# Optimization experiments

Measured on AMD Instinct MI355X. Metric: run time of the kernel, lower is better.

The kernel has to match this reference:

```python
import jax, jax.numpy as jnp
import numpy as np

B, H, S, D = 2, 16, 2048, 64

def setup_inputs() -> dict:
    key = jax.random.key(0)
    kq, kk, kv = jax.random.split(key, 3)
    q = jax.random.normal(kq, (B, H, S, D), dtype=jnp.float32)
    k = jax.random.normal(kk, (B, H, S, D), dtype=jnp.float32)
    v = jax.random.normal(kv, (B, H, S, D), dtype=jnp.float32)
    # causal mask: True where position j > i (future tokens are masked)
    mask = jnp.triu(jnp.ones((S, S), dtype=bool), k=1)[None, None, :, :]
    return {"q": q, "k": k, "v": v, "mask": mask}

def reference(q, k, v, mask) -> jnp.ndarray:
    # scaled dot-product attention with additive -1e4 mask bias
    scale = 1.0 / jnp.sqrt(jnp.asarray(q.shape[-1], q.dtype))
    scores = jnp.einsum('bhqd,bhkd->bhqk', q, k) * scale  # [B,H,S,S]
    scores = scores + mask.astype(scores.dtype) * jnp.asarray(-10000.0, scores.dtype)
    probs = jax.nn.softmax(scores, axis=-1)
    # dropout is identity in eval mode
    return jnp.einsum('bhqk,bhkd->bhqd', probs, v)
```

## Files before the change

kernel.cpp:

```cpp
#include <hip/hip_runtime.h>

typedef __bf16 bf16_t;
typedef bf16_t bf16x2 __attribute__((ext_vector_type(2)));
typedef bf16_t bf16x4 __attribute__((ext_vector_type(4)));
typedef bf16_t bf16x8 __attribute__((ext_vector_type(8)));
typedef float  floatx16 __attribute__((ext_vector_type(16)));
typedef unsigned int uintx4 __attribute__((ext_vector_type(4)));

constexpr int Sq = 2048, Dq = 64;
constexpr int BQ = 128;
constexpr int KVB = 64;
constexpr int NQT = Sq / BQ;
constexpr float SCALE_LOG2E = 0.125f * 1.44269504088896340736f;

struct LoopS { bf16_t K[2][2][KVB * Dq]; bf16_t V[2][2][Dq * KVB]; };
struct EpiS  { float Op[BQ][Dq]; float den[BQ]; };
union  SmemU { LoopS l; EpiS e; };

static __device__ __forceinline__ bf16x8 cvt8(const float4& a, const float4& b) {
    bf16x8 w;
    w[0] = (bf16_t)a.x; w[1] = (bf16_t)a.y; w[2] = (bf16_t)a.z; w[3] = (bf16_t)a.w;
    w[4] = (bf16_t)b.x; w[5] = (bf16_t)b.y; w[6] = (bf16_t)b.z; w[7] = (bf16_t)b.w;
    return w;
}
static __device__ __forceinline__ bf16x8 cvt8s(const float4& a, const float4& b) {
    bf16x8 w;
    w[0] = (bf16_t)(a.x * SCALE_LOG2E); w[1] = (bf16_t)(a.y * SCALE_LOG2E);
    w[2] = (bf16_t)(a.z * SCALE_LOG2E); w[3] = (bf16_t)(a.w * SCALE_LOG2E);
    w[4] = (bf16_t)(b.x * SCALE_LOG2E); w[5] = (bf16_t)(b.y * SCALE_LOG2E);
    w[6] = (bf16_t)(b.z * SCALE_LOG2E); w[7] = (bf16_t)(b.w * SCALE_LOG2E);
    return w;
}
static __device__ __forceinline__ unsigned int pkbf(float lo, float hi) {
    bf16x2 t; t[0] = (bf16_t)lo; t[1] = (bf16_t)hi;
    return __builtin_bit_cast(unsigned int, t);
}

#define SUM16(p) (((((p)[0]+(p)[1])+((p)[2]+(p)[3]))+(((p)[4]+(p)[5])+((p)[6]+(p)[7]))) \
                + ((((p)[8]+(p)[9])+((p)[10]+(p)[11]))+(((p)[12]+(p)[13])+((p)[14]+(p)[15]))))

#define LOADKV(kt) do {                                                        \
    const long kb_ = base + (long)(kt) * KVB * Dq;                             \
    const float* ks_ = &K[kb_ + (long)krow_st * Dq + kd0];                     \
    kr0 = *(const float4*)&ks_[0];  kr1 = *(const float4*)&ks_[4];             \
    kr2 = *(const float4*)&ks_[8];  kr3 = *(const float4*)&ks_[12];            \
    _Pragma("unroll")                                                          \
    for (int p_ = 0; p_ < 4; ++p_) {                                           \
        const int j0_ = vjw + 4 * ((p_ + vh) & 3);                             \
        _Pragma("unroll")                                                      \
        for (int r_ = 0; r_ < 4; ++r_)                                         \
            vraw[p_][r_] = V[kb_ + (long)(j0_ + r_) * Dq + vd];                \
    } } while (0)

#define WRITEKV(kdst, vdst) do {                                               \
    char* kc_ = (char*)(kdst) + krow_st * 128;                                 \
    const int ksw_ = (krow_st & 7) << 4;                                       \
    *(bf16x8*)(kc_ + ((2 * kd0) ^ ksw_))      = cvt8(kr0, kr1);                \
    *(bf16x8*)(kc_ + ((2 * kd0 + 16) ^ ksw_)) = cvt8(kr2, kr3);                \
    char* vc_ = (char*)(vdst) + vd * 128;                                      \
    const int vsw_ = (vd & 7) << 4;                                            \
    _Pragma("unroll")                                                          \
    for (int p_ = 0; p_ < 4; ++p_) {                                           \
        const int j0_ = vjw + 4 * ((p_ + vh) & 3);                             \
        bf16x4 vw_;                                                            \
        vw_[0] = (bf16_t)vraw[p_][0]; vw_[1] = (bf16_t)vraw[p_][1];            \
        vw_[2] = (bf16_t)vraw[p_][2]; vw_[3] = (bf16_t)vraw[p_][3];            \
        *(bf16x4*)(vc_ + ((2 * j0_) ^ vsw_)) = vw_;                            \
    } } while (0)

__global__ __launch_bounds__(512, 2) void flash_attn_kernel(
    const float* __restrict__ Q, const float* __restrict__ K,
    const float* __restrict__ V, float* __restrict__ O)
{
    __shared__ SmemU sm;

    const int tid  = threadIdx.x;
    const int grp  = tid >> 8;
    const int gtid = tid & 255;
    const int wave = gtid >> 6;
    const int lane = gtid & 63;
    const int hi   = lane >> 5;
    const int l31  = lane & 31;

    const int id = blockIdx.x;
    const int bh = (id & 7) + ((id >> 6) << 3);
    const int pr = (id >> 3) & 7;
    const long base = (long)bh * Sq * Dq;

    const int krow_st = gtid >> 2;
    const int kd0     = 16 * (gtid & 3);
    const int vd      = gtid & 63;
    const int vjw     = 16 * (gtid >> 6);
    const int vh      = (gtid & 63) >> 3;

    bf16_t* const Kb0 = &sm.l.K[grp][0][0];
    bf16_t* const Kb1 = &sm.l.K[grp][1][0];
    bf16_t* const Vb0 = &sm.l.V[grp][0][0];
    bf16_t* const Vb1 = &sm.l.V[grp][1][0];
    const int lsw = (l31 & 7) << 4;

    for (int half = 0; half < 2; ++half) {
        const int qt = half ? (NQT - 1 - pr) : pr;
        const long qb = base + (long)qt * BQ * Dq;
        const int qrow = 32 * wave + l31;
        const int niter = qt + 1;

        bf16x8 qf[4];
        #pragma unroll
        for (int ss = 0; ss < 4; ++ss) {
            const float* qp = &Q[qb + (long)qrow * Dq + 16 * ss + 8 * hi];
            qf[ss] = cvt8s(*(const float4*)&qp[0], *(const float4*)&qp[4]);
        }

        float4 kr0, kr1, kr2, kr3;
        float  vraw[4][4];

        __syncthreads();
        LOADKV(grp);
        WRITEKV(Kb0, Vb0);
        __syncthreads();

        float l_lane = 0.f;
        floatx16 oacc[2];
        oacc[0] = (floatx16)0.f; oacc[1] = (floatx16)0.f;

        for (int i = 0; i < niter; ++i) {
            const int kt = 2 * i + grp;
            const bool more = (i + 1 < niter);
            if (more) LOADKV(kt + 2);

            if (64 * kt <= BQ * qt + 32 * wave + 31) {
                const bf16_t* kbase = (i & 1) ? Kb1 : Kb0;
                const bf16_t* vbase = (i & 1) ? Vb1 : Vb0;

                floatx16 s0 = (floatx16)0.f, s1 = (floatx16)0.f;
                __builtin_amdgcn_s_setprio(1);
                #pragma unroll
                for (int ss = 0; ss < 4; ++ss) {
                    const int cb = (32 * ss + 16 * hi) ^ lsw;
                    bf16x8 k0 = *(const bf16x8*)((const char*)kbase + l31 * 128 + cb);
                    bf16x8 k1 = *(const bf16x8*)((const char*)kbase + (32 + l31) * 128 + cb);
                    s0 = __builtin_amdgcn_mfma_f32_32x32x16_bf16(k0, qf[ss], s0, 0, 0, 0);
                    s1 = __builtin_amdgcn_mfma_f32_32x32x16_bf16(k1, qf[ss], s1, 0, 0, 0);
                }
                __builtin_amdgcn_s_setprio(0);

                float p0[16], p1[16];
                const bool diag = (kt >= 2 * qt);
                const int kg0 = 64 * kt;
                const int qg  = BQ * qt + qrow;
                #pragma unroll
                for (int r = 0; r < 16; ++r) {
                    const int cr = (r & 3) + 8 * (r >> 2) + 4 * hi;
                    float a = s0[r], b = s1[r];
                    if (diag) {
                        if (kg0 + cr > qg)      a = -1e30f;
                        if (kg0 + 32 + cr > qg) b = -1e30f;
                    }
                    p0[r] = __builtin_amdgcn_exp2f(a);
                    p1[r] = __builtin_amdgcn_exp2f(b);
                }
                l_lane += SUM16(p0) + SUM16(p1);

                unsigned int w[4][4];
                #pragma unroll
                for (int s = 0; s < 4; ++s) {
                    const float* pt = (s >> 1) ? p1 : p0;
                    const int R = 8 * (s & 1);
                    unsigned int c0 = pkbf(pt[R + 0], pt[R + 1]);
                    unsigned int c1 = pkbf(pt[R + 2], pt[R + 3]);
                    unsigned int d0 = pkbf(pt[R + 4], pt[R + 5]);
                    unsigned int d1 = pkbf(pt[R + 6], pt[R + 7]);
                    asm volatile("v_permlane32_swap_b32 %0, %1" : "+v"(c0), "+v"(d0));
                    asm volatile("v_permlane32_swap_b32 %0, %1" : "+v"(c1), "+v"(d1));
                    w[s][0] = c0; w[s][1] = c1; w[s][2] = d0; w[s][3] = d1;
                }

                __builtin_amdgcn_s_setprio(1);
                #pragma unroll
                for (int t2 = 0; t2 < 2; ++t2) {
                    #pragma unroll
                    for (int s = 0; s < 4; ++s) {
                        uintx4 fw; fw[0] = w[s][0]; fw[1] = w[s][1];
                        fw[2] = w[s][2]; fw[3] = w[s][3];
                        const bf16x8 pa = __builtin_bit_cast(bf16x8, fw);
                        const int cb = (32 * s + 16 * hi) ^ lsw;
                        bf16x8 vf = *(const bf16x8*)((const char*)vbase + (32 * t2 + l31) * 128 + cb);
                        oacc[t2] = __builtin_amdgcn_mfma_f32_32x32x16_bf16(pa, vf, oacc[t2], 0, 0, 0);
                    }
                }
                __builtin_amdgcn_s_setprio(0);
            }

            if (more) WRITEKV((i & 1) ? Kb0 : Kb1, (i & 1) ? Vb0 : Vb1);
            __syncthreads();
        }

        const float lden = l_lane + __shfl_xor(l_lane, 32);

        if (grp == 1) {
            #pragma unroll
            for (int t2 = 0; t2 < 2; ++t2)
                #pragma unroll
                for (int r = 0; r < 16; ++r) {
                    const int cr = (r & 3) + 8 * (r >> 2) + 4 * hi;
                    sm.e.Op[32 * wave + cr][32 * t2 + l31] = oacc[t2][r];
                }
            if (hi == 0) sm.e.den[32 * wave + l31] = lden;
        }
        __syncthreads();
        if (grp == 0) {
            #pragma unroll
            for (int r = 0; r < 16; ++r) {
                const int cr = (r & 3) + 8 * (r >> 2) + 4 * hi;
                const float dA = __shfl(lden, cr);
                const float dB = sm.e.den[32 * wave + cr];
                const float inv = 1.f / (dA + dB);
                const long orow = qb + (long)(32 * wave + cr) * Dq;
                #pragma unroll
                for (int t2 = 0; t2 < 2; ++t2) {
                    const float ov = oacc[t2][r] + sm.e.Op[32 * wave + cr][32 * t2 + l31];
                    O[orow + 32 * t2 + l31] = ov * inv;
                }
            }
        }
    }
}

extern "C" void kernel_launch(void* const* d_in, const int* in_sizes, int n_in,
                              void* d_out, int out_size, void* d_ws, size_t ws_size,
                              hipStream_t stream)
{
    const float* q = (const float*)d_in[0];
    const float* k = (const float*)d_in[1];
    const float* v = (const float*)d_in[2];
    float* out = (float*)d_out;
    flash_attn_kernel<<<dim3(256, 1, 1), dim3(512, 1, 1), 0, stream>>>(q, k, v, out);
}
```

Measured before the change: 143.8 us.

## Halve query and KV tile sizes and double grid with padded V layout

Shrinks the query tile from 128 to 64 rows and the KV tile from 64 to 32, launching 512 blocks of 256 threads instead of 256 blocks of 512. V is now stored transposed in shared memory with an 80-byte padded row stride instead of the XOR swizzle, so each thread writes 16 contiguous bf16 values with two vector stores. The aim is more blocks for load balance across CUs and a simpler V staging path. The cost is lower per-block MFMA reuse, twice as many barriers per unit of work, and less work between synchronisations.

```diff
diff --git a/kernel.cpp b/kernel.cpp
--- a/kernel.cpp
+++ b/kernel.cpp
@@ -2,18 +2,19 @@
 
 typedef __bf16 bf16_t;
 typedef bf16_t bf16x2 __attribute__((ext_vector_type(2)));
-typedef bf16_t bf16x4 __attribute__((ext_vector_type(4)));
 typedef bf16_t bf16x8 __attribute__((ext_vector_type(8)));
 typedef float  floatx16 __attribute__((ext_vector_type(16)));
 typedef unsigned int uintx4 __attribute__((ext_vector_type(4)));
 
 constexpr int Sq = 2048, Dq = 64;
-constexpr int BQ = 128;
-constexpr int KVB = 64;
+constexpr int BQ = 64;
+constexpr int KVB = 32;
 constexpr int NQT = Sq / BQ;
 constexpr float SCALE_LOG2E = 0.125f * 1.44269504088896340736f;
-
-struct LoopS { bf16_t K[2][2][KVB * Dq]; bf16_t V[2][2][Dq * KVB]; };
+constexpr int KROW_B = 128;
+constexpr int VROW_B = 80;
+
+struct LoopS { char Kl[2][2][KVB * KROW_B]; char Vl[2][2][Dq * VROW_B]; };
 struct EpiS  { float Op[BQ][Dq]; float den[BQ]; };
 union  SmemU { LoopS l; EpiS e; };
 
@@ -39,160 +40,148 @@
 #define SUM16(p) (((((p)[0]+(p)[1])+((p)[2]+(p)[3]))+(((p)[4]+(p)[5])+((p)[6]+(p)[7]))) \
                 + ((((p)[8]+(p)[9])+((p)[10]+(p)[11]))+(((p)[12]+(p)[13])+((p)[14]+(p)[15]))))
 
-#define LOADKV(kt) do {                                                        \
-    const long kb_ = base + (long)(kt) * KVB * Dq;                             \
-    const float* ks_ = &K[kb_ + (long)krow_st * Dq + kd0];                     \
-    kr0 = *(const float4*)&ks_[0];  kr1 = *(const float4*)&ks_[4];             \
-    kr2 = *(const float4*)&ks_[8];  kr3 = *(const float4*)&ks_[12];            \
+#define LOADKV(TG) do {                                                        \
+    const long kb_ = base + (long)(TG) * KVB * Dq;                             \
+    const float* kp_ = &K[kb_ + (long)krow_l * Dq + kc0];                      \
+    kr0 = *(const float4*)&kp_[0];  kr1 = *(const float4*)&kp_[4];             \
+    kr2 = *(const float4*)&kp_[8];  kr3 = *(const float4*)&kp_[12];            \
+    const float* vp_ = &V[kb_ + (long)(16 * vkh) * Dq + vd];                   \
     _Pragma("unroll")                                                          \
-    for (int p_ = 0; p_ < 4; ++p_) {                                           \
-        const int j0_ = vjw + 4 * ((p_ + vh) & 3);                             \
-        _Pragma("unroll")                                                      \
-        for (int r_ = 0; r_ < 4; ++r_)                                         \
-            vraw[p_][r_] = V[kb_ + (long)(j0_ + r_) * Dq + vd];                \
-    } } while (0)
-
-#define WRITEKV(kdst, vdst) do {                                               \
-    char* kc_ = (char*)(kdst) + krow_st * 128;                                 \
-    const int ksw_ = (krow_st & 7) << 4;                                       \
-    *(bf16x8*)(kc_ + ((2 * kd0) ^ ksw_))      = cvt8(kr0, kr1);                \
-    *(bf16x8*)(kc_ + ((2 * kd0 + 16) ^ ksw_)) = cvt8(kr2, kr3);                \
-    char* vc_ = (char*)(vdst) + vd * 128;                                      \
-    const int vsw_ = (vd & 7) << 4;                                            \
+    for (int m_ = 0; m_ < 16; ++m_) vraw[m_] = vp_[m_ * Dq];                   \
+} while (0)
+
+#define WRITEKV(BUF) do {                                                      \
+    char* kc_ = &sm.l.Kl[grp][BUF][krow_l * KROW_B];                           \
+    const int ksw_ = (krow_l & 7) << 4;                                        \
+    *(bf16x8*)(kc_ + ((2 * kc0) ^ ksw_))      = cvt8(kr0, kr1);                \
+    *(bf16x8*)(kc_ + ((2 * kc0 + 16) ^ ksw_)) = cvt8(kr2, kr3);                \
+    char* vc_ = &sm.l.Vl[grp][BUF][vd * VROW_B + 32 * vkh];                    \
+    bf16x8 v0_, v1_;                                                           \
     _Pragma("unroll")                                                          \
-    for (int p_ = 0; p_ < 4; ++p_) {                                           \
-        const int j0_ = vjw + 4 * ((p_ + vh) & 3);                             \
-        bf16x4 vw_;                                                            \
-        vw_[0] = (bf16_t)vraw[p_][0]; vw_[1] = (bf16_t)vraw[p_][1];            \
-        vw_[2] = (bf16_t)vraw[p_][2]; vw_[3] = (bf16_t)vraw[p_][3];            \
-        *(bf16x4*)(vc_ + ((2 * j0_) ^ vsw_)) = vw_;                            \
-    } } while (0)
-
-__global__ __launch_bounds__(512, 2) void flash_attn_kernel(
+    for (int m_ = 0; m_ < 8; ++m_) {                                           \
+        v0_[m_] = (bf16_t)vraw[m_]; v1_[m_] = (bf16_t)vraw[8 + m_];            \
+    }                                                                          \
+    *(bf16x8*)(vc_)      = v0_;                                                \
+    *(bf16x8*)(vc_ + 16) = v1_;                                                \
+} while (0)
+
+__global__ __launch_bounds__(256, 2) void flash_attn_kernel(
     const float* __restrict__ Q, const float* __restrict__ K,
     const float* __restrict__ V, float* __restrict__ O)
 {
     __shared__ SmemU sm;
 
     const int tid  = threadIdx.x;
-    const int grp  = tid >> 8;
-    const int gtid = tid & 255;
-    const int wave = gtid >> 6;
-    const int lane = gtid & 63;
+    const int wave = tid >> 6;
+    const int lane = tid & 63;
     const int hi   = lane >> 5;
     const int l31  = lane & 31;
+    const int grp  = wave >> 1;
+    const int qh   = wave & 1;
 
     const int id = blockIdx.x;
-    const int bh = (id & 7) + ((id >> 6) << 3);
-    const int pr = (id >> 3) & 7;
+    const int bh = (id & 7) + ((id >> 7) << 3);
+    const int pr = (id >> 3) & 15;
     const long base = (long)bh * Sq * Dq;
 
-    const int krow_st = gtid >> 2;
-    const int kd0     = 16 * (gtid & 3);
-    const int vd      = gtid & 63;
-    const int vjw     = 16 * (gtid >> 6);
-    const int vh      = (gtid & 63) >> 3;
-
-    bf16_t* const Kb0 = &sm.l.K[grp][0][0];
-    bf16_t* const Kb1 = &sm.l.K[grp][1][0];
-    bf16_t* const Vb0 = &sm.l.V[grp][0][0];
-    bf16_t* const Vb1 = &sm.l.V[grp][1][0];
-    const int lsw = (l31 & 7) << 4;
+    const int gt     = tid & 127;
+    const int krow_l = gt >> 2;
+    const int kc0    = (gt & 3) * 16;
+    const int vd     = gt >> 1;
+    const int vkh    = gt & 1;
 
     for (int half = 0; half < 2; ++half) {
         const int qt = half ? (NQT - 1 - pr) : pr;
         const long qb = base + (long)qt * BQ * Dq;
-        const int qrow = 32 * wave + l31;
-        const int niter = qt + 1;
-
-        bf16x8 qf[4];
-        #pragma unroll
-        for (int ss = 0; ss < 4; ++ss) {
-            const float* qp = &Q[qb + (long)qrow * Dq + 16 * ss + 8 * hi];
-            qf[ss] = cvt8s(*(const float4*)&qp[0], *(const float4*)&qp[4]);
+
+        bf16x8 qf0, qf1, qf2, qf3;
+        {
+            const float* qp = &Q[qb + (long)(32 * qh + l31) * Dq + 8 * hi];
+            qf0 = cvt8s(*(const float4*)&qp[0],  *(const float4*)&qp[4]);
+            qf1 = cvt8s(*(const float4*)&qp[16], *(const float4*)&qp[20]);
+            qf2 = cvt8s(*(const float4*)&qp[32], *(const float4*)&qp[36]);
+            qf3 = cvt8s(*(const float4*)&qp[48], *(const float4*)&qp[52]);
         }
 
         float4 kr0, kr1, kr2, kr3;
-        float  vraw[4][4];
+        float  vraw[16];
+        float  l_lane = 0.f;
+        floatx16 oacc0 = (floatx16)0.f, oacc1 = (floatx16)0.f;
 
         __syncthreads();
         LOADKV(grp);
-        WRITEKV(Kb0, Vb0);
+        WRITEKV(0);
         __syncthreads();
 
-        float l_lane = 0.f;
-        floatx16 oacc[2];
-        oacc[0] = (floatx16)0.f; oacc[1] = (floatx16)0.f;
-
-        for (int i = 0; i < niter; ++i) {
-            const int kt = 2 * i + grp;
-            const bool more = (i + 1 < niter);
-            if (more) LOADKV(kt + 2);
-
-            if (64 * kt <= BQ * qt + 32 * wave + 31) {
-                const bf16_t* kbase = (i & 1) ? Kb1 : Kb0;
-                const bf16_t* vbase = (i & 1) ? Vb1 : Vb0;
-
-                floatx16 s0 = (floatx16)0.f, s1 = (floatx16)0.f;
+        for (int s = 0; s <= qt; ++s) {
+            const int buf = s & 1;
+            const bool more = (s < qt);
+            if (more) LOADKV(2 * (s + 1) + grp);
+
+            const int tg = 2 * s + grp;
+            if (32 * tg <= 64 * qt + 32 * qh + 31) {
+                const char* kb_ = &sm.l.Kl[grp][buf][l31 * KROW_B];
+                const int lsw = (l31 & 7) << 4;
+
+                floatx16 s0 = (floatx16)0.f;
                 __builtin_amdgcn_s_setprio(1);
-                #pragma unroll
-                for (int ss = 0; ss < 4; ++ss) {
-                    const int cb = (32 * ss + 16 * hi) ^ lsw;
-                    bf16x8 k0 = *(const bf16x8*)((const char*)kbase + l31 * 128 + cb);
-                    bf16x8 k1 = *(const bf16x8*)((const char*)kbase + (32 + l31) * 128 + cb);
-                    s0 = __builtin_amdgcn_mfma_f32_32x32x16_bf16(k0, qf[ss], s0, 0, 0, 0);
-                    s1 = __builtin_amdgcn_mfma_f32_32x32x16_bf16(k1, qf[ss], s1, 0, 0, 0);
-                }
+                s0 = __builtin_amdgcn_mfma_f32_32x32x16_bf16(
+                         *(const bf16x8*)(kb_ + ((16 * hi) ^ lsw)),      qf0, s0, 0, 0, 0);
+                s0 = __builtin_amdgcn_mfma_f32_32x32x16_bf16(
+                         *(const bf16x8*)(kb_ + ((32 + 16 * hi) ^ lsw)), qf1, s0, 0, 0, 0);
+                s0 = __builtin_amdgcn_mfma_f32_32x32x16_bf16(
+                         *(const bf16x8*)(kb_ + ((64 + 16 * hi) ^ lsw)), qf2, s0, 0, 0, 0);
+                s0 = __builtin_amdgcn_mfma_f32_32x32x16_bf16(
+                         *(const bf16x8*)(kb_ + ((96 + 16 * hi) ^ lsw)), qf3, s0, 0, 0, 0);
                 __builtin_amdgcn_s_setprio(0);
 
-                float p0[16], p1[16];
-                const bool diag = (kt >= 2 * qt);
-                const int kg0 = 64 * kt;
-                const int qg  = BQ * qt + qrow;
+                float p0[16];
+                const bool diag = (tg == 2 * qt + qh);
                 #pragma unroll
                 for (int r = 0; r < 16; ++r) {
                     const int cr = (r & 3) + 8 * (r >> 2) + 4 * hi;
-                    float a = s0[r], b = s1[r];
-                    if (diag) {
-                        if (kg0 + cr > qg)      a = -1e30f;
-                        if (kg0 + 32 + cr > qg) b = -1e30f;
-                    }
+                    float a = s0[r];
+                    if (diag && (32 * tg + cr > 64 * qt + 32 * qh + l31)) a = -1e30f;
                     p0[r] = __builtin_amdgcn_exp2f(a);
-                    p1[r] = __builtin_amdgcn_exp2f(b);
                 }
-                l_lane += SUM16(p0) + SUM16(p1);
-
-                unsigned int w[4][4];
-                #pragma unroll
-                for (int s = 0; s < 4; ++s) {
-                    const float* pt = (s >> 1) ? p1 : p0;
-                    const int R = 8 * (s & 1);
-                    unsigned int c0 = pkbf(pt[R + 0], pt[R + 1]);
-                    unsigned int c1 = pkbf(pt[R + 2], pt[R + 3]);
-                    unsigned int d0 = pkbf(pt[R + 4], pt[R + 5]);
-                    unsigned int d1 = pkbf(pt[R + 6], pt[R + 7]);
+                l_lane += SUM16(p0);
+
+                unsigned int w00, w01, w02, w03, w10, w11, w12, w13;
+                {
+                    unsigned int c0 = pkbf(p0[0], p0[1]), c1 = pkbf(p0[2], p0[3]);
+                    unsigned int d0 = pkbf(p0[4], p0[5]), d1 = pkbf(p0[6], p0[7]);
                     asm volatile("v_permlane32_swap_b32 %0, %1" : "+v"(c0), "+v"(d0));
                     asm volatile("v_permlane32_swap_b32 %0, %1" : "+v"(c1), "+v"(d1));
-                    w[s][0] = c0; w[s][1] = c1; w[s][2] = d0; w[s][3] = d1;
+                    w00 = c0; w01 = c1; w02 = d0; w03 = d1;
                 }
-
+                {
+                    unsigned int c0 = pkbf(p0[8], p0[9]),   c1 = pkbf(p0[10], p0[11]);
+                    unsigned int d0 = pkbf(p0[12], p0[13]), d1 = pkbf(p0[14], p0[15]);
+                    asm volatile("v_permlane32_swap_b32 %0, %1" : "+v"(c0), "+v"(d0));
+                    asm volatile("v_permlane32_swap_b32 %0, %1" : "+v"(c1), "+v"(d1));
+                    w10 = c0; w11 = c1; w12 = d0; w13 = d1;
+                }
+                uintx4 f0; f0[0] = w00; f0[1] = w01; f0[2] = w02; f0[3] = w03;
+                uintx4 f1; f1[0] = w10; f1[1] = w11; f1[2] = w12; f1[3] = w13;
+                const bf16x8 pa0 = __builtin_bit_cast(bf16x8, f0);
+                const bf16x8 pa1 = __builtin_bit_cast(bf16x8, f1);
+
+                const char* vb_ = &sm.l.Vl[grp][buf][0];
+                const char* vr0 = vb_ + l31 * VROW_B + 16 * hi;
+                const char* vr1 = vb_ + (32 + l31) * VROW_B + 16 * hi;
                 __builtin_amdgcn_s_setprio(1);
-                #pragma unroll
-                for (int t2 = 0; t2 < 2; ++t2) {
-                    #pragma unroll
-                    for (int s = 0; s < 4; ++s) {
-                        uintx4 fw; fw[0] = w[s][0]; fw[1] = w[s][1];
-                        fw[2] = w[s][2]; fw[3] = w[s][3];
-                        const bf16x8 pa = __builtin_bit_cast(bf16x8, fw);
-                        const int cb = (32 * s + 16 * hi) ^ lsw;
-                        bf16x8 vf = *(const bf16x8*)((const char*)vbase + (32 * t2 + l31) * 128 + cb);
-                        oacc[t2] = __builtin_amdgcn_mfma_f32_32x32x16_bf16(pa, vf, oacc[t2], 0, 0, 0);
-                    }
-                }
+                oacc0 = __builtin_amdgcn_mfma_f32_32x32x16_bf16(
+                            pa0, *(const bf16x8*)(vr0),      oacc0, 0, 0, 0);
+                oacc0 = __builtin_amdgcn_mfma_f32_32x32x16_bf16(
+                            pa1, *(const bf16x8*)(vr0 + 32), oacc0, 0, 0, 0);
+                oacc1 = __builtin_amdgcn_mfma_f32_32x32x16_bf16(
+                            pa0, *(const bf16x8*)(vr1),      oacc1, 0, 0, 0);
+                oacc1 = __builtin_amdgcn_mfma_f32_32x32x16_bf16(
+                            pa1, *(const bf16x8*)(vr1 + 32), oacc1, 0, 0, 0);
                 __builtin_amdgcn_s_setprio(0);
             }
 
-            if (more) WRITEKV((i & 1) ? Kb0 : Kb1, (i & 1) ? Vb0 : Vb1);
+            if (more) WRITEKV(buf ^ 1);
             __syncthreads();
         }
 
@@ -200,13 +189,12 @@
 
         if (grp == 1) {
             #pragma unroll
-            for (int t2 = 0; t2 < 2; ++t2)
-                #pragma unroll
-                for (int r = 0; r < 16; ++r) {
-                    const int cr = (r & 3) + 8 * (r >> 2) + 4 * hi;
-                    sm.e.Op[32 * wave + cr][32 * t2 + l31] = oacc[t2][r];
-                }
-            if (hi == 0) sm.e.den[32 * wave + l31] = lden;
+            for (int r = 0; r < 16; ++r) {
+                const int cr = (r & 3) + 8 * (r >> 2) + 4 * hi;
+                sm.e.Op[32 * qh + cr][l31]      = oacc0[r];
+                sm.e.Op[32 * qh + cr][32 + l31] = oacc1[r];
+            }
+            if (hi == 0) sm.e.den[32 * qh + l31] = lden;
         }
         __syncthreads();
         if (grp == 0) {
@@ -214,14 +202,11 @@
             for (int r = 0; r < 16; ++r) {
                 const int cr = (r & 3) + 8 * (r >> 2) + 4 * hi;
                 const float dA = __shfl(lden, cr);
-                const float dB = sm.e.den[32 * wave + cr];
+                const float dB = sm.e.den[32 * qh + cr];
                 const float inv = 1.f / (dA + dB);
-                const long orow = qb + (long)(32 * wave + cr) * Dq;
-                #pragma unroll
-                for (int t2 = 0; t2 < 2; ++t2) {
-                    const float ov = oacc[t2][r] + sm.e.Op[32 * wave + cr][32 * t2 + l31];
-                    O[orow + 32 * t2 + l31] = ov * inv;
-                }
+                const long orow = qb + (long)(32 * qh + cr) * Dq;
+                O[orow + l31]      = (oacc0[r] + sm.e.Op[32 * qh + cr][l31]) * inv;
+                O[orow + 32 + l31] = (oacc1[r] + sm.e.Op[32 * qh + cr][32 + l31]) * inv;
             }
         }
     }
@@ -235,5 +220,5 @@
     const float* k = (const float*)d_in[1];
     const float* v = (const float*)d_in[2];
     float* out = (float*)d_out;
-    flash_attn_kernel<<<dim3(256, 1, 1), dim3(512, 1, 1), 0, stream>>>(q, k, v, out);
-}
+    flash_attn_kernel<<<dim3(512, 1, 1), dim3(256, 1, 1), 0, stream>>>(q, k, v, out);
+}
```

Result: slower. 147.6 us (+2.7%).
